# Performance work log

Measured on AMD Instinct MI355X. Metric: run time of the kernel, lower is better.

## Reference

```python
import jax, jax.numpy as jnp
import numpy as np

N_STATES = 256  # uint8 accumulator state space
N_VALS = 256    # uint8 quantized input values


def setup_inputs() -> dict:
    key = jax.random.key(0)
    k1, k2, k3 = jax.random.split(key, 3)
    B, C, O = 8192, 64, 128
    x = jax.random.randint(k1, (B, C, O), 0, N_VALS, dtype=jnp.int32)
    # per-output-position state transition tables: add_table[j][state, byte] -> new state
    add_table = jax.random.randint(k2, (O, N_STATES, N_VALS), 0, N_STATES, dtype=jnp.int32)
    # final lookup table: softmax_table[state, byte] -> output value
    softmax_table = jax.random.uniform(k3, (N_STATES, N_VALS), dtype=jnp.float32)
    return {"x": x, "add_table": add_table, "softmax_table": softmax_table}


def reference(x, add_table, softmax_table):
    # x: [B, C, O] int32 in [0, 256)
    # add_table: [O, S, 256] int32 (state transitions), softmax_table: [S, 256] float32
    B, C, O = x.shape
    xT = jnp.transpose(x, (2, 0, 1))  # [O, B, C] for scanning over output positions

    def step(state, inputs):
        xj, tab = inputs                 # xj: [B, C], tab: [S, 256]
        new_state = tab[state, xj]       # vectorized gather over batch & channels
        return new_state, None

    s0 = jnp.zeros((B, C), dtype=jnp.int32)
    s_final, _ = jax.lax.scan(step, s0, (xT, add_table))  # s_final: [B, C]

    # final per-element lookup conditioned on accumulated state
    out = softmax_table[s_final[:, :, None], x]  # [B, C, O]
    return out
```

## Files before the change

kernel.cpp:

```cpp
#include <hip/hip_runtime.h>


constexpr int O_DIM = 128;
constexpr long long NCHAINS = 8192LL * 64;
constexpr int TAB_ENTRIES = 128 * 256 * 256;

constexpr size_t WS_S    = 8u << 20;
constexpr size_t WS_PX   = 16u << 20;
constexpr size_t WS_FULL = 80u << 20;
constexpr size_t WS_MID  = 12u << 20;

typedef int   vi4 __attribute__((ext_vector_type(4)));
typedef float vf4 __attribute__((ext_vector_type(4)));

__global__ __launch_bounds__(256)
void pack_kernel(const int* __restrict__ t32, unsigned char* __restrict__ t8) {
    const int i = (blockIdx.x * 256 + threadIdx.x) * 4;
    vi4 v = *reinterpret_cast<const vi4*>(t32 + i);
    unsigned b = ((unsigned)v.x & 0xffu) | (((unsigned)v.y & 0xffu) << 8) |
                 (((unsigned)v.z & 0xffu) << 16) | (((unsigned)v.w & 0xffu) << 24);
    *reinterpret_cast<unsigned*>(t8 + i) = b;
}

constexpr int WBLK = 1024;
constexpr int WCH  = 2048;

template <int WRITE_PX>
__global__ __launch_bounds__(WBLK, 4)
void walk_kernel(const int* __restrict__ x, const unsigned char* __restrict__ t8,
                 int* __restrict__ s_out, unsigned* __restrict__ gpx) {
    __shared__ unsigned char slice[2][65536];
    unsigned* pxw = reinterpret_cast<unsigned*>(&slice[0][0]);

    const int t = threadIdx.x;
    const size_t chain0 = (size_t)blockIdx.x * WCH;

    unsigned px0[32], px1[32];

    auto window = [&](int h, unsigned (&dst)[32]) {
        const vi4* xv = reinterpret_cast<const vi4*>(x + (chain0 + (size_t)h * 1024) * O_DIM);
#pragma unroll 4
        for (int k = 0; k < 32; ++k) {
            const int idx = k * WBLK + t;
            vi4 v = __builtin_nontemporal_load(&xv[idx]);
            unsigned p = (unsigned)v.x | ((unsigned)v.y << 8) |
                         ((unsigned)v.z << 16) | ((unsigned)v.w << 24);
            const int cl = idx >> 5;
            const int d  = idx & 31;
            pxw[cl * 32 + (d ^ (cl & 31))] = p;
        }
        __syncthreads();
#pragma unroll
        for (int k = 0; k < 32; ++k)
            dst[k] = pxw[t * 32 + (k ^ (t & 31))];
        if (WRITE_PX) {
            unsigned* gp = gpx + (chain0 + (size_t)h * 1024) * 32;
#pragma unroll 4
            for (int q = 0; q < 32; ++q) {
                const int idx = q * WBLK + t;
                const int cl = idx >> 5;
                const int d  = idx & 31;
                __builtin_nontemporal_store(pxw[cl * 32 + (d ^ (cl & 31))], &gp[idx]);
            }
        }
        __syncthreads();
    };
    window(0, px0);
    window(1, px1);

    auto stage = [&](int j, int b) {
        const unsigned char* gsrc = t8 + ((size_t)j << 16);
#pragma unroll
        for (int r = 0; r < 4; ++r) {
            __builtin_amdgcn_global_load_lds(
                (const __attribute__((address_space(1))) void*)(gsrc + r * 16384 + t * 16),
                (__attribute__((address_space(3))) void*)(&slice[b][r * 16384 + t * 16]),
                16, 0, 0);
        }
    };

    stage(0, 0);
    asm volatile("s_waitcnt vmcnt(0)" ::: "memory");
    __builtin_amdgcn_s_barrier();

    int s0 = 0, s1 = 0;
#pragma unroll
    for (int j = 0; j < 127; ++j) {
        stage(j + 1, (j + 1) & 1);
        asm volatile("s_waitcnt vmcnt(4)" ::: "memory");
        __builtin_amdgcn_s_barrier();
        const int buf = j & 1;
        const unsigned xb0 = (px0[j >> 2] >> ((j & 3) * 8)) & 0xffu;
        const unsigned xb1 = (px1[j >> 2] >> ((j & 3) * 8)) & 0xffu;
        s0 = slice[buf][((unsigned)s0 << 8) | xb0];
        s1 = slice[buf][((unsigned)s1 << 8) | xb1];
        asm volatile("s_waitcnt lgkmcnt(0)" ::: "memory");
        __builtin_amdgcn_s_barrier();
    }
    asm volatile("s_waitcnt vmcnt(0)" ::: "memory");
    __builtin_amdgcn_s_barrier();
    {
        const unsigned xb0 = px0[31] >> 24;
        const unsigned xb1 = px1[31] >> 24;
        s0 = slice[1][((unsigned)s0 << 8) | xb0];
        s1 = slice[1][((unsigned)s1 << 8) | xb1];
    }

    s_out[chain0 + t]        = s0;
    s_out[chain0 + 1024 + t] = s1;
}

constexpr int BBLK = 512;
constexpr int CPB_B = 128;
constexpr int GRID_B = 256;
constexpr int CHUNKS = (int)(NCHAINS / ((long long)GRID_B * CPB_B));

__device__ __forceinline__ unsigned short f2bf(float f) {
    unsigned b = __float_as_uint(f);
    return (unsigned short)((b + 0x7fffu + ((b >> 16) & 1u)) >> 16);
}
__device__ __forceinline__ float bf2f(unsigned short h) {
    return __uint_as_float(((unsigned)h) << 16);
}

template <int PX_U8>
__global__ __launch_bounds__(BBLK)
void out_kernel(const int* __restrict__ x, const unsigned* __restrict__ gpx,
                const int* __restrict__ s_in, const float* __restrict__ st,
                float* __restrict__ out) {
    __shared__ unsigned short st_l[65536];
    __shared__ unsigned px_l[CPB_B * 32];
    __shared__ int s_l[CPB_B];
    const int t = threadIdx.x;

    const vf4* stv = reinterpret_cast<const vf4*>(st);
    unsigned* stl32 = reinterpret_cast<unsigned*>(st_l);
#pragma unroll 4
    for (int k = 0; k < 32; ++k) {
        const int idx = k * BBLK + t;
        vf4 v = stv[idx];
        unsigned w0 = (unsigned)f2bf(v.x) | ((unsigned)f2bf(v.y) << 16);
        unsigned w1 = (unsigned)f2bf(v.z) | ((unsigned)f2bf(v.w) << 16);
        stl32[idx * 2]     = w0;
        stl32[idx * 2 + 1] = w1;
    }
    __syncthreads();

    for (int c = 0; c < CHUNKS; ++c) {
        const size_t chain0 = ((size_t)blockIdx.x * CHUNKS + c) * CPB_B;

        if (PX_U8) {
#pragma unroll
            for (int k = 0; k < 8; ++k) {
                const int idx = k * BBLK + t;
                px_l[idx] = __builtin_nontemporal_load(&gpx[chain0 * 32 + idx]);
            }
        } else {
            const vi4* xv = reinterpret_cast<const vi4*>(x + chain0 * O_DIM);
#pragma unroll
            for (int k = 0; k < 8; ++k) {
                const int idx = k * BBLK + t;
                vi4 v = __builtin_nontemporal_load(&xv[idx]);
                px_l[idx] = (unsigned)v.x | ((unsigned)v.y << 8) |
                            ((unsigned)v.z << 16) | ((unsigned)v.w << 24);
            }
        }
        if (t < CPB_B) s_l[t] = s_in[chain0 + t];
        __syncthreads();

        vf4* ov = reinterpret_cast<vf4*>(out + chain0 * O_DIM);
#pragma unroll 2
        for (int k = 0; k < 8; ++k) {
            const int idx = k * BBLK + t;
            unsigned p = px_l[idx];
            const int row = s_l[idx >> 5] << 8;
            vf4 r;
            r.x = bf2f(st_l[row + (p & 0xffu)]);
            r.y = bf2f(st_l[row + ((p >> 8) & 0xffu)]);
            r.z = bf2f(st_l[row + ((p >> 16) & 0xffu)]);
            r.w = bf2f(st_l[row + (p >> 24)]);
            __builtin_nontemporal_store(r, &ov[idx]);
        }
        __syncthreads();
    }
}

__global__ __launch_bounds__(128)
void fused_kernel(const int* __restrict__ x, const int* __restrict__ add_table,
                  const float* __restrict__ st, float* __restrict__ out) {
    __shared__ unsigned px_lds[128 * 32];
    __shared__ int s_lds[128];
    const int t = threadIdx.x;
    const size_t chain0 = (size_t)blockIdx.x * 128;
    const vi4* xv = reinterpret_cast<const vi4*>(x + chain0 * O_DIM);
#pragma unroll 4
    for (int k = 0; k < 32; ++k) {
        const int idx = k * 128 + t;
        vi4 v = __builtin_nontemporal_load(&xv[idx]);
        unsigned p = (unsigned)v.x | ((unsigned)v.y << 8) |
                     ((unsigned)v.z << 16) | ((unsigned)v.w << 24);
        px_lds[(idx >> 5) * 32 + ((idx & 31) ^ ((idx >> 5) & 31))] = p;
    }
    __syncthreads();
    unsigned px[32];
#pragma unroll
    for (int k = 0; k < 32; ++k) px[k] = px_lds[t * 32 + (k ^ (t & 31))];
    int s = 0;
#pragma unroll
    for (int j = 0; j < O_DIM; ++j) {
        unsigned xj = (px[j >> 2] >> ((j & 3) * 8)) & 0xffu;
        s = add_table[((unsigned)j << 16) | ((unsigned)s << 8) | xj];
    }
    s_lds[t] = s;
    __syncthreads();
    vf4* ov = reinterpret_cast<vf4*>(out + chain0 * O_DIM);
#pragma unroll 4
    for (int k = 0; k < 32; ++k) {
        const int idx = k * 128 + t;
        const int chain = idx >> 5, q = idx & 31;
        unsigned p = px_lds[chain * 32 + (q ^ (chain & 31))];
        const float* row = st + ((unsigned)s_lds[chain] << 8);
        vf4 r;
        r.x = row[p & 0xffu]; r.y = row[(p >> 8) & 0xffu];
        r.z = row[(p >> 16) & 0xffu]; r.w = row[p >> 24];
        __builtin_nontemporal_store(r, &ov[idx]);
    }
}

extern "C" void kernel_launch(void* const* d_in, const int* in_sizes, int n_in,
                              void* d_out, int out_size, void* d_ws, size_t ws_size,
                              hipStream_t stream) {
    const int* x         = (const int*)d_in[0];
    const int* add_table = (const int*)d_in[1];
    const float* st      = (const float*)d_in[2];
    float* out           = (float*)d_out;
    char* ws             = (char*)d_ws;

    if (ws_size >= WS_FULL) {
        unsigned char* t8 = (unsigned char*)ws;
        int* s_ws    = (int*)(ws + WS_S);
        unsigned* px = (unsigned*)(ws + WS_PX);
        pack_kernel<<<TAB_ENTRIES / 4 / 256, 256, 0, stream>>>(add_table, t8);
        walk_kernel<1><<<(int)(NCHAINS / WCH), WBLK, 0, stream>>>(x, t8, s_ws, px);
        out_kernel<1><<<GRID_B, BBLK, 0, stream>>>(x, px, s_ws, st, out);
    } else if (ws_size >= WS_MID) {
        unsigned char* t8 = (unsigned char*)ws;
        int* s_ws = (int*)(ws + WS_S);
        pack_kernel<<<TAB_ENTRIES / 4 / 256, 256, 0, stream>>>(add_table, t8);
        walk_kernel<0><<<(int)(NCHAINS / WCH), WBLK, 0, stream>>>(x, t8, s_ws, nullptr);
        out_kernel<0><<<GRID_B, BBLK, 0, stream>>>(x, nullptr, s_ws, st, out);
    } else {
        fused_kernel<<<(int)(NCHAINS / 128), 128, 0, stream>>>(x, add_table, st, out);
    }
}
```

Measured before the change: 203.5 us.

## Fuse state walk and output lookup into one kernel keeping packed inputs in registers

Merges the walk kernel and the output kernel into one kernel. After the 128-step state walk, each block reuses its LDS as a bf16 copy of the softmax table and writes outputs straight from the packed x bytes and final states it already holds in registers. This removes the global round trips for the packed x array and the final-state buffer, and drops one kernel launch. In exchange, each of the 256 blocks reloads and converts the full softmax table, and the output phase adds eight extra barrier-separated chunk stages per window.

```diff
diff --git a/kernel.cpp b/kernel.cpp
--- a/kernel.cpp
+++ b/kernel.cpp
@@ -4,11 +4,6 @@
 constexpr int O_DIM = 128;
 constexpr long long NCHAINS = 8192LL * 64;
 constexpr int TAB_ENTRIES = 128 * 256 * 256;
-
-constexpr size_t WS_S    = 8u << 20;
-constexpr size_t WS_PX   = 16u << 20;
-constexpr size_t WS_FULL = 80u << 20;
-constexpr size_t WS_MID  = 12u << 20;
 
 typedef int   vi4 __attribute__((ext_vector_type(4)));
 typedef float vf4 __attribute__((ext_vector_type(4)));
@@ -22,14 +17,23 @@
     *reinterpret_cast<unsigned*>(t8 + i) = b;
 }
 
+__device__ __forceinline__ unsigned f2bf(float f) {
+    unsigned b = __float_as_uint(f);
+    return (b + 0x7fffu + ((b >> 16) & 1u)) >> 16;
+}
+__device__ __forceinline__ float bf2f(unsigned short h) {
+    return __uint_as_float(((unsigned)h) << 16);
+}
+
 constexpr int WBLK = 1024;
 constexpr int WCH  = 2048;
 
-template <int WRITE_PX>
 __global__ __launch_bounds__(WBLK, 4)
-void walk_kernel(const int* __restrict__ x, const unsigned char* __restrict__ t8,
-                 int* __restrict__ s_out, unsigned* __restrict__ gpx) {
+void fused_ws(const int* __restrict__ x, const unsigned char* __restrict__ t8,
+              const float* __restrict__ st, float* __restrict__ out) {
     __shared__ unsigned char slice[2][65536];
+    __shared__ unsigned px_out[128 * 32];
+    __shared__ int s_l[128];
     unsigned* pxw = reinterpret_cast<unsigned*>(&slice[0][0]);
 
     const int t = threadIdx.x;
@@ -53,16 +57,6 @@
 #pragma unroll
         for (int k = 0; k < 32; ++k)
             dst[k] = pxw[t * 32 + (k ^ (t & 31))];
-        if (WRITE_PX) {
-            unsigned* gp = gpx + (chain0 + (size_t)h * 1024) * 32;
-#pragma unroll 4
-            for (int q = 0; q < 32; ++q) {
-                const int idx = q * WBLK + t;
-                const int cl = idx >> 5;
-                const int d  = idx & 31;
-                __builtin_nontemporal_store(pxw[cl * 32 + (d ^ (cl & 31))], &gp[idx]);
-            }
-        }
         __syncthreads();
     };
     window(0, px0);
@@ -105,84 +99,50 @@
         s0 = slice[1][((unsigned)s0 << 8) | xb0];
         s1 = slice[1][((unsigned)s1 << 8) | xb1];
     }
-
-    s_out[chain0 + t]        = s0;
-    s_out[chain0 + 1024 + t] = s1;
-}
-
-constexpr int BBLK = 512;
-constexpr int CPB_B = 128;
-constexpr int GRID_B = 256;
-constexpr int CHUNKS = (int)(NCHAINS / ((long long)GRID_B * CPB_B));
-
-__device__ __forceinline__ unsigned short f2bf(float f) {
-    unsigned b = __float_as_uint(f);
-    return (unsigned short)((b + 0x7fffu + ((b >> 16) & 1u)) >> 16);
-}
-__device__ __forceinline__ float bf2f(unsigned short h) {
-    return __uint_as_float(((unsigned)h) << 16);
-}
-
-template <int PX_U8>
-__global__ __launch_bounds__(BBLK)
-void out_kernel(const int* __restrict__ x, const unsigned* __restrict__ gpx,
-                const int* __restrict__ s_in, const float* __restrict__ st,
-                float* __restrict__ out) {
-    __shared__ unsigned short st_l[65536];
-    __shared__ unsigned px_l[CPB_B * 32];
-    __shared__ int s_l[CPB_B];
-    const int t = threadIdx.x;
-
+    __syncthreads();
+
+    unsigned* stl32 = reinterpret_cast<unsigned*>(&slice[0][0]);
+    unsigned short* st_l = reinterpret_cast<unsigned short*>(&slice[0][0]);
     const vf4* stv = reinterpret_cast<const vf4*>(st);
-    unsigned* stl32 = reinterpret_cast<unsigned*>(st_l);
-#pragma unroll 4
-    for (int k = 0; k < 32; ++k) {
-        const int idx = k * BBLK + t;
+#pragma unroll 4
+    for (int k = 0; k < 16; ++k) {
+        const int idx = k * WBLK + t;
         vf4 v = stv[idx];
-        unsigned w0 = (unsigned)f2bf(v.x) | ((unsigned)f2bf(v.y) << 16);
-        unsigned w1 = (unsigned)f2bf(v.z) | ((unsigned)f2bf(v.w) << 16);
-        stl32[idx * 2]     = w0;
-        stl32[idx * 2 + 1] = w1;
-    }
-    __syncthreads();
-
-    for (int c = 0; c < CHUNKS; ++c) {
-        const size_t chain0 = ((size_t)blockIdx.x * CHUNKS + c) * CPB_B;
-
-        if (PX_U8) {
-#pragma unroll
-            for (int k = 0; k < 8; ++k) {
-                const int idx = k * BBLK + t;
-                px_l[idx] = __builtin_nontemporal_load(&gpx[chain0 * 32 + idx]);
+        stl32[idx * 2]     = f2bf(v.x) | (f2bf(v.y) << 16);
+        stl32[idx * 2 + 1] = f2bf(v.z) | (f2bf(v.w) << 16);
+    }
+    __syncthreads();
+
+    auto do_chunks = [&](const unsigned (&pp)[32], int sreg, int w) {
+        for (int c = 0; c < 8; ++c) {
+            if ((t >> 7) == c) {
+                const int lc = t & 127;
+                s_l[lc] = sreg;
+#pragma unroll
+                for (int k = 0; k < 32; ++k)
+                    px_out[lc * 32 + (k ^ (lc & 31))] = pp[k];
             }
-        } else {
-            const vi4* xv = reinterpret_cast<const vi4*>(x + chain0 * O_DIM);
-#pragma unroll
-            for (int k = 0; k < 8; ++k) {
-                const int idx = k * BBLK + t;
-                vi4 v = __builtin_nontemporal_load(&xv[idx]);
-                px_l[idx] = (unsigned)v.x | ((unsigned)v.y << 8) |
-                            ((unsigned)v.z << 16) | ((unsigned)v.w << 24);
+            __syncthreads();
+            vf4* ov = reinterpret_cast<vf4*>(
+                out + (chain0 + (size_t)w * 1024 + (size_t)c * 128) * O_DIM);
+#pragma unroll
+            for (int k = 0; k < 4; ++k) {
+                const int idx = k * WBLK + t;
+                const int cl = idx >> 5, q = idx & 31;
+                unsigned p = px_out[cl * 32 + (q ^ (cl & 31))];
+                const int row = s_l[cl] << 8;
+                vf4 r;
+                r.x = bf2f((unsigned short)st_l[row + (p & 0xffu)]);
+                r.y = bf2f((unsigned short)st_l[row + ((p >> 8) & 0xffu)]);
+                r.z = bf2f((unsigned short)st_l[row + ((p >> 16) & 0xffu)]);
+                r.w = bf2f((unsigned short)st_l[row + (p >> 24)]);
+                __builtin_nontemporal_store(r, &ov[idx]);
             }
+            __syncthreads();
         }
-        if (t < CPB_B) s_l[t] = s_in[chain0 + t];
-        __syncthreads();
-
-        vf4* ov = reinterpret_cast<vf4*>(out + chain0 * O_DIM);
-#pragma unroll 2
-        for (int k = 0; k < 8; ++k) {
-            const int idx = k * BBLK + t;
-            unsigned p = px_l[idx];
-            const int row = s_l[idx >> 5] << 8;
-            vf4 r;
-            r.x = bf2f(st_l[row + (p & 0xffu)]);
-            r.y = bf2f(st_l[row + ((p >> 8) & 0xffu)]);
-            r.z = bf2f(st_l[row + ((p >> 16) & 0xffu)]);
-            r.w = bf2f(st_l[row + (p >> 24)]);
-            __builtin_nontemporal_store(r, &ov[idx]);
-        }
-        __syncthreads();
-    }
+    };
+    do_chunks(px0, s0, 0);
+    do_chunks(px1, s1, 1);
 }
 
 __global__ __launch_bounds__(128)
@@ -234,21 +194,11 @@
     const int* add_table = (const int*)d_in[1];
     const float* st      = (const float*)d_in[2];
     float* out           = (float*)d_out;
-    char* ws             = (char*)d_ws;
-
-    if (ws_size >= WS_FULL) {
-        unsigned char* t8 = (unsigned char*)ws;
-        int* s_ws    = (int*)(ws + WS_S);
-        unsigned* px = (unsigned*)(ws + WS_PX);
+
+    if (ws_size >= (size_t)TAB_ENTRIES) {
+        unsigned char* t8 = (unsigned char*)d_ws;
         pack_kernel<<<TAB_ENTRIES / 4 / 256, 256, 0, stream>>>(add_table, t8);
-        walk_kernel<1><<<(int)(NCHAINS / WCH), WBLK, 0, stream>>>(x, t8, s_ws, px);
-        out_kernel<1><<<GRID_B, BBLK, 0, stream>>>(x, px, s_ws, st, out);
-    } else if (ws_size >= WS_MID) {
-        unsigned char* t8 = (unsigned char*)ws;
-        int* s_ws = (int*)(ws + WS_S);
-        pack_kernel<<<TAB_ENTRIES / 4 / 256, 256, 0, stream>>>(add_table, t8);
-        walk_kernel<0><<<(int)(NCHAINS / WCH), WBLK, 0, stream>>>(x, t8, s_ws, nullptr);
-        out_kernel<0><<<GRID_B, BBLK, 0, stream>>>(x, nullptr, s_ws, st, out);
+        fused_ws<<<(int)(NCHAINS / WCH), WBLK, 0, stream>>>(x, t8, st, out);
     } else {
         fused_kernel<<<(int)(NCHAINS / 128), 128, 0, stream>>>(x, add_table, st, out);
     }
```

After: 185.2 us. 9.0% less time.
